# Kernel tuning notes

Measured on AMD Instinct MI355X. Metric: run time of the kernel, lower is better.

Reference implementation:

```python
import jax, jax.numpy as jnp
import numpy as np

NUM_HEADS = 16


def setup_inputs() -> dict:
    key = jax.random.key(0)
    ks = jax.random.split(key, 5)
    B, N, C = 4, 2048, 1024
    x = jax.random.normal(ks[0], (B, N, C), dtype=jnp.float32)
    mask = jax.random.randint(ks[1], (B, N), 0, 2, dtype=jnp.int32)
    W_qkv = jax.random.normal(ks[2], (C, 3 * C), dtype=jnp.float32) * (C ** -0.5)
    W_proj = jax.random.normal(ks[3], (C, C), dtype=jnp.float32) * (C ** -0.5)
    b_proj = jnp.zeros((C,), dtype=jnp.float32)
    return {"x": x, "mask": mask, "W_qkv": W_qkv, "W_proj": W_proj, "b_proj": b_proj}


def reference(x, mask, W_qkv, W_proj, b_proj):
    B, N, C = x.shape
    H = NUM_HEADS
    hd = C // H
    scale = hd ** -0.5
    # qkv projection -> [3, B, H, N, hd]
    qkv = (x @ W_qkv).reshape(B, N, 3, H, hd).transpose(2, 0, 3, 1, 4)
    q, k, v = qkv[0], qkv[1], qkv[2]
    attn = jnp.einsum('bhqd,bhkd->bhqk', q, k) * scale  # [B,H,N,N]
    add_mask = (mask[:, None, None, :] != 1).astype(jnp.float32) * -10000.0
    attn = jax.nn.softmax(attn + add_mask, axis=-1)
    out = jnp.einsum('bhqk,bhkd->bhqd', attn, v)  # [B,H,N,hd]
    out = out.transpose(0, 2, 1, 3).reshape(B, N, C)
    return out @ W_proj + b_proj
```

## Files before the change

### kernel.cpp

```cpp
#include <hip/hip_runtime.h>

typedef unsigned short u16;
typedef unsigned int u32;
typedef unsigned long long u64;
typedef __attribute__((ext_vector_type(8))) short short8;
typedef __attribute__((ext_vector_type(4))) float f32x4;

#define MLOGC (-14426.95f)

__device__ __forceinline__ u16 f2bf(float f) {
  u32 u = __builtin_bit_cast(u32, f);
  u += 0x7fffu + ((u >> 16) & 1u);
  return (u16)(u >> 16);
}

__device__ __forceinline__ float fexp2(float x) {
#if __has_builtin(__builtin_amdgcn_exp2f)
  return __builtin_amdgcn_exp2f(x);
#else
  return exp2f(x);
#endif
}

__device__ __forceinline__ void glds16(u16* lds, const u16* g) {
  __builtin_amdgcn_global_load_lds(
      (const __attribute__((address_space(1))) u32*)g,
      (__attribute__((address_space(3))) u32*)lds, 16, 0, 0);
}

#define MFMA(a, b, c) __builtin_amdgcn_mfma_f32_16x16x32_bf16((a), (b), (c), 0, 0, 0)


__global__ __launch_bounds__(256) void prep(const float* __restrict__ x,
                                            const int* __restrict__ mask,
                                            const float* __restrict__ Wqkv,
                                            const float* __restrict__ Wproj,
                                            u16* __restrict__ xb,
                                            u16* __restrict__ wqkvt,
                                            u16* __restrict__ wprojt,
                                            int* __restrict__ s2t,
                                            int* __restrict__ nkbuf) {
  __shared__ float tile[64][65];
  __shared__ int wtot[4];
  __shared__ int wbase[5];
  const int bid = blockIdx.x, t = threadIdx.x;

  if (bid < 8192) {
    int i = bid * 256 + t;
    float4 v = ((const float4*)x)[i];
    union { u16 s[4]; u64 ll; } u;
    u.s[0] = f2bf(v.x); u.s[1] = f2bf(v.y); u.s[2] = f2bf(v.z); u.s[3] = f2bf(v.w);
    ((u64*)xb)[i] = u.ll;
    return;
  }
  if (bid < 9216) {
    const float* Wm; u16* Wt; int Cc, bj, bi;
    if (bid < 8960) { int tt = bid - 8192; Wm = Wqkv;  Wt = wqkvt;  Cc = 3072; bj = tt % 48; bi = tt / 48; }
    else            { int tt = bid - 8960; Wm = Wproj; Wt = wprojt; Cc = 1024; bj = tt & 15; bi = tt >> 4; }
    const int r = t >> 4, c4 = (t & 15) << 2;
    for (int rr = r; rr < 64; rr += 16) {
      float4 v = *(const float4*)&Wm[(size_t)(bi * 64 + rr) * Cc + bj * 64 + c4];
      tile[rr][c4] = v.x; tile[rr][c4 + 1] = v.y; tile[rr][c4 + 2] = v.z; tile[rr][c4 + 3] = v.w;
    }
    __syncthreads();
    for (int rr = r; rr < 64; rr += 16) {
      union { u16 s[4]; u64 ll; } u;
      u.s[0] = f2bf(tile[c4][rr]);
      u.s[1] = f2bf(tile[c4 + 1][rr]);
      u.s[2] = f2bf(tile[c4 + 2][rr]);
      u.s[3] = f2bf(tile[c4 + 3][rr]);
      *(u64*)&Wt[(size_t)(bj * 64 + rr) * 1024 + bi * 64 + c4] = u.ll;
    }
    return;
  }
  const int b = bid - 9216;
  const int lane = t & 63, w = t >> 6;
  int m8[8], c = 0;
  #pragma unroll
  for (int j = 0; j < 8; j++) {
    m8[j] = (mask[b * 2048 + t * 8 + j] == 1);
    c += m8[j];
  }
  int incl = c;
  #pragma unroll
  for (int off = 1; off < 64; off <<= 1) {
    int v = __shfl_up(incl, off);
    if (lane >= off) incl += v;
  }
  if (lane == 63) wtot[w] = incl;
  __syncthreads();
  if (t == 0) {
    int s = 0;
    for (int i = 0; i < 4; i++) { wbase[i] = s; s += wtot[i]; }
    wbase[4] = s;
  }
  __syncthreads();
  const int nk = wbase[4];
  int urun = wbase[w] + incl - c;
  #pragma unroll
  for (int j = 0; j < 8; j++) {
    int tok = t * 8 + j;
    int slot = m8[j] ? urun : nk + (tok - urun);
    s2t[b * 2048 + slot] = b * 2048 + tok;
    urun += m8[j];
  }
  if (t == 0) nkbuf[b] = nk;
}

__global__ __launch_bounds__(256, 4) void gemm_fused(const u16* __restrict__ xb,
                                                     const u16* __restrict__ wqkvt,
                                                     const int* __restrict__ s2t,
                                                     const int* __restrict__ nkbuf,
                                                     u16* __restrict__ qbuf,
                                                     u16* __restrict__ kc,
                                                     u16* __restrict__ vtc) {
  __shared__ u16 Asm[128 * 64];
  __shared__ u16 Bsm[128 * 64];
  const int bid = blockIdx.x;
  const int role = bid >> 9;
  const int sub = bid & 511;
  const int tid = threadIdx.x, lane = tid & 63, w = tid >> 6;
  const int quad = lane >> 4, l15 = lane & 15;
  const int wm = (w >> 1) * 64, wn = (w & 1) * 64;
  const int srow = lane >> 3;
  const int gcc = ((lane & 7) ^ srow) * 8;
  const int rx8 = (l15 & 7);

  int m0, n0;
  const u16 *Asrc, *Bsrc;
  if (role == 2) { m0 = (sub & 7) * 128; n0 = (sub >> 3) * 128; }
  else           { m0 = (sub >> 3) * 128; n0 = (sub & 7) * 128; }
  if (role == 1 && (m0 & 2047) >= nkbuf[m0 >> 11]) return;
  if (role == 2 && (n0 & 2047) >= nkbuf[n0 >> 11]) return;

  int arow[4], brow[4];
  #pragma unroll
  for (int c = 0; c < 4; ++c) {
    int rit = (w * 4 + c) * 8 + srow;
    if (role == 0)      { arow[c] = m0 + rit;            brow[c] = n0 + rit; }
    else if (role == 1) { arow[c] = s2t[m0 + rit];       brow[c] = 1024 + n0 + rit; }
    else                { arow[c] = 2048 + m0 + rit;     brow[c] = s2t[n0 + rit]; }
  }
  Asrc = (role == 2) ? wqkvt : xb;
  Bsrc = (role == 2) ? xb : wqkvt;

  f32x4 acc[4][4];
  #pragma unroll
  for (int i = 0; i < 4; i++)
    #pragma unroll
    for (int j = 0; j < 4; j++)
      #pragma unroll
      for (int r = 0; r < 4; r++) acc[i][j][r] = 0.f;

  for (int kt = 0; kt < 1024; kt += 64) {
    __syncthreads();
    #pragma unroll
    for (int c = 0; c < 4; ++c) {
      int chunk = w * 4 + c;
      glds16(&Asm[chunk * 512], &Asrc[(size_t)arow[c] * 1024 + kt + gcc]);
      glds16(&Bsm[chunk * 512], &Bsrc[(size_t)brow[c] * 1024 + kt + gcc]);
    }
    __syncthreads();
    #pragma unroll
    for (int ks = 0; ks < 2; ++ks) {
      int pc = ((ks * 4 + quad) ^ rx8) * 8;
      short8 av[4], bv[4];
      #pragma unroll
      for (int i = 0; i < 4; i++)
        av[i] = *(const short8*)&Asm[(wm + i * 16 + l15) * 64 + pc];
      #pragma unroll
      for (int j = 0; j < 4; j++)
        bv[j] = *(const short8*)&Bsm[(wn + j * 16 + l15) * 64 + pc];
      #pragma unroll
      for (int i = 0; i < 4; i++)
        #pragma unroll
        for (int j = 0; j < 4; j++)
          acc[i][j] = MFMA(av[i], bv[j], acc[i][j]);
    }
  }

  if (role == 2) {
    #pragma unroll
    for (int j = 0; j < 4; j++) {
      int col = n0 + wn + j * 16 + l15;
      int bb = col >> 11, sl = col & 2047;
      #pragma unroll
      for (int i = 0; i < 4; i++)
        #pragma unroll
        for (int r = 0; r < 4; r++) {
          int row = m0 + wm + i * 16 + quad * 4 + r;
          vtc[(size_t)(bb * 1024 + row) * 2048 + sl] = f2bf(acc[i][j][r]);
        }
    }
  } else {
    u16* dst = (role == 0) ? qbuf : kc;
    #pragma unroll
    for (int i = 0; i < 4; i++)
      #pragma unroll
      for (int j = 0; j < 4; j++) {
        int col = n0 + wn + j * 16 + l15;
        #pragma unroll
        for (int r = 0; r < 4; r++) {
          int row = m0 + wm + i * 16 + quad * 4 + r;
          dst[(size_t)row * 1024 + col] = f2bf(acc[i][j][r]);
        }
      }
  }
}

__global__ __launch_bounds__(256, 2) void attn_kernel(const u16* __restrict__ q,
                                                      const u16* __restrict__ kc,
                                                      const u16* __restrict__ vtc,
                                                      const int* __restrict__ nkbuf,
                                                      u16* __restrict__ ao) {
  __shared__ u16 Ksm[64 * 64];
  __shared__ u16 Vsm[64 * 64];
  __shared__ u16 Psm[4 * 64 * 72];
  const int h = blockIdx.x, b = blockIdx.y, qt = blockIdx.z;
  const int tid = threadIdx.x, lane = tid & 63, w = tid >> 6;
  const int quad = lane >> 4, l15 = lane & 15;
  const int q0 = qt * 256 + w * 64;
  const int srow = lane >> 3;
  const int gcc = ((lane & 7) ^ srow) * 8;
  const int rx8 = (l15 & 7);
  const float C1 = 0.18033688f;
  const int nk = nkbuf[b];
  const int ntiles = (nk + 63) >> 6;

  short8 qf[4][2];
  #pragma unroll
  for (int i = 0; i < 4; i++)
    #pragma unroll
    for (int ks = 0; ks < 2; ks++)
      qf[i][ks] = *(const short8*)&q[(size_t)(b * 2048 + q0 + i * 16 + l15) * 1024 +
                                     h * 64 + ks * 32 + quad * 8];

  f32x4 o[4][4];
  float lsum[4][4];
  #pragma unroll
  for (int i = 0; i < 4; i++)
    #pragma unroll
    for (int r = 0; r < 4; r++) {
      lsum[i][r] = 0.f;
      #pragma unroll
      for (int jd = 0; jd < 4; jd++) o[i][jd][r] = 0.f;
    }

  for (int t = 0; t < ntiles; ++t) {
    const int k0 = t * 64;
    __syncthreads();
    #pragma unroll
    for (int c = 0; c < 2; ++c) {
      int chunk = w * 2 + c;
      int r = chunk * 8 + srow;
      glds16(&Ksm[chunk * 512], &kc[(size_t)(b * 2048 + k0 + r) * 1024 + h * 64 + gcc]);
      glds16(&Vsm[chunk * 512], &vtc[(size_t)(b * 1024 + h * 64 + r) * 2048 + k0 + gcc]);
    }
    __syncthreads();

    f32x4 s[4][4];
    #pragma unroll
    for (int i = 0; i < 4; i++)
      #pragma unroll
      for (int j = 0; j < 4; j++)
        #pragma unroll
        for (int r = 0; r < 4; r++) s[i][j][r] = 0.f;
    #pragma unroll
    for (int ks = 0; ks < 2; ks++) {
      int pc = ((ks * 4 + quad) ^ rx8) * 8;
      short8 kf[4];
      #pragma unroll
      for (int j = 0; j < 4; j++)
        kf[j] = *(const short8*)&Ksm[(j * 16 + l15) * 64 + pc];
      #pragma unroll
      for (int i = 0; i < 4; i++)
        #pragma unroll
        for (int j = 0; j < 4; j++) s[i][j] = MFMA(qf[i][ks], kf[j], s[i][j]);
    }

    float mlog[4];
    #pragma unroll
    for (int j = 0; j < 4; j++)
      mlog[j] = (k0 + j * 16 + l15 < nk) ? 0.f : MLOGC;

    #pragma unroll
    for (int i = 0; i < 4; i++) {
      #pragma unroll
      for (int r = 0; r < 4; r++) {
        int prow = i * 16 + quad * 4 + r;
        float ps = 0.f;
        #pragma unroll
        for (int j = 0; j < 4; j++) {
          float p = fexp2(__builtin_fmaf(s[i][j][r], C1, mlog[j]));
          ps += p;
          u32 pv = __builtin_bit_cast(u32, p) + 0x8000u;
          Psm[w * 4608 + prow * 72 + j * 16 + l15] = ((const u16*)&pv)[1];
        }
        lsum[i][r] += ps;
      }
    }

    #pragma unroll
    for (int ks = 0; ks < 2; ks++) {
      int pcv = ((ks * 4 + quad) ^ rx8) * 8;
      int kk = ks * 32 + quad * 8;
      short8 pf[4], vf[4];
      #pragma unroll
      for (int i = 0; i < 4; i++)
        pf[i] = *(const short8*)&Psm[w * 4608 + (i * 16 + l15) * 72 + kk];
      #pragma unroll
      for (int jd = 0; jd < 4; jd++)
        vf[jd] = *(const short8*)&Vsm[(jd * 16 + l15) * 64 + pcv];
      #pragma unroll
      for (int i = 0; i < 4; i++)
        #pragma unroll
        for (int jd = 0; jd < 4; jd++) o[i][jd] = MFMA(pf[i], vf[jd], o[i][jd]);
    }
  }

  #pragma unroll
  for (int i = 0; i < 4; i++)
    #pragma unroll
    for (int r = 0; r < 4; r++) {
      float l = lsum[i][r];
      #pragma unroll
      for (int off = 8; off >= 1; off >>= 1) l += __shfl_xor(l, off);
      float inv = 1.f / l;
      size_t row = (size_t)(b * 2048 + q0 + i * 16 + quad * 4 + r);
      #pragma unroll
      for (int jd = 0; jd < 4; jd++)
        ao[row * 1024 + h * 64 + jd * 16 + l15] = f2bf(o[i][jd][r] * inv);
    }
}

__global__ __launch_bounds__(256, 3) void gemm_proj(const u16* __restrict__ A,
                                                    const u16* __restrict__ Bt,
                                                    const float* __restrict__ bias,
                                                    float* __restrict__ out) {
  __shared__ u16 Asm[128 * 64];
  __shared__ u16 Bsm[128 * 64];
  const int tid = threadIdx.x, lane = tid & 63, w = tid >> 6;
  const int quad = lane >> 4, l15 = lane & 15;
  const int m0 = blockIdx.y * 128, n0 = blockIdx.x * 128;
  const int wm = (w >> 1) * 64, wn = (w & 1) * 64;
  const int srow = lane >> 3;
  const int gcc = ((lane & 7) ^ srow) * 8;
  const int rx8 = (l15 & 7);
  f32x4 acc[4][4];
  #pragma unroll
  for (int i = 0; i < 4; i++)
    #pragma unroll
    for (int j = 0; j < 4; j++)
      #pragma unroll
      for (int r = 0; r < 4; r++) acc[i][j][r] = 0.f;

  for (int kt = 0; kt < 1024; kt += 64) {
    __syncthreads();
    #pragma unroll
    for (int c = 0; c < 4; ++c) {
      int chunk = w * 4 + c;
      int row = chunk * 8 + srow;
      glds16(&Asm[chunk * 512], &A[(size_t)(m0 + row) * 1024 + kt + gcc]);
      glds16(&Bsm[chunk * 512], &Bt[(size_t)(n0 + row) * 1024 + kt + gcc]);
    }
    __syncthreads();
    #pragma unroll
    for (int ks = 0; ks < 2; ++ks) {
      int pc = ((ks * 4 + quad) ^ rx8) * 8;
      short8 av[4], bv[4];
      #pragma unroll
      for (int i = 0; i < 4; i++)
        av[i] = *(const short8*)&Asm[(wm + i * 16 + l15) * 64 + pc];
      #pragma unroll
      for (int j = 0; j < 4; j++)
        bv[j] = *(const short8*)&Bsm[(wn + j * 16 + l15) * 64 + pc];
      #pragma unroll
      for (int i = 0; i < 4; i++)
        #pragma unroll
        for (int j = 0; j < 4; j++)
          acc[i][j] = MFMA(av[i], bv[j], acc[i][j]);
    }
  }

  #pragma unroll
  for (int j = 0; j < 4; j++) {
    int col = n0 + wn + j * 16 + l15;
    float bj = bias[col];
    #pragma unroll
    for (int i = 0; i < 4; i++) {
      #pragma unroll
      for (int r = 0; r < 4; r++) {
        int row = m0 + wm + i * 16 + quad * 4 + r;
        out[(size_t)row * 1024 + col] = acc[i][j][r] + bj;
      }
    }
  }
}

extern "C" void kernel_launch(void* const* d_in, const int* in_sizes, int n_in,
                              void* d_out, int out_size, void* d_ws, size_t ws_size,
                              hipStream_t stream) {
  (void)in_sizes; (void)n_in; (void)out_size; (void)ws_size;
  const float* x     = (const float*)d_in[0];
  const int*   mask  = (const int*)d_in[1];
  const float* Wqkv  = (const float*)d_in[2];
  const float* Wproj = (const float*)d_in[3];
  const float* bproj = (const float*)d_in[4];
  float* out = (float*)d_out;
  char* ws = (char*)d_ws;

  size_t off = 0;
  u16* xb     = (u16*)(ws + off); off += 8192ull * 1024 * 2;
  u16* wqkvt  = (u16*)(ws + off); off += 3072ull * 1024 * 2;
  u16* wprojt = (u16*)(ws + off); off += 1024ull * 1024 * 2;
  u16* qbuf   = (u16*)(ws + off); off += 8192ull * 1024 * 2;
  u16* kcbuf  = (u16*)(ws + off); off += 4096ull * 2048 * 2;
  u16* vtcbuf = (u16*)(ws + off); off += 4096ull * 2048 * 2;
  u16* aobuf  = (u16*)(ws + off); off += 8192ull * 1024 * 2;
  int* s2t    = (int*)(ws + off); off += 8192ull * 4;
  int* nkbuf  = (int*)(ws + off); off += 4 * 4;

  prep<<<9220, 256, 0, stream>>>(x, mask, Wqkv, Wproj, xb, wqkvt, wprojt, s2t, nkbuf);
  gemm_fused<<<1536, 256, 0, stream>>>(xb, wqkvt, s2t, nkbuf, qbuf, kcbuf, vtcbuf);
  attn_kernel<<<dim3(16, 4, 8), 256, 0, stream>>>(qbuf, kcbuf, vtcbuf, nkbuf, aobuf);
  gemm_proj<<<dim3(8, 64), 256, 0, stream>>>(aobuf, wprojt, bproj, out);
}
```

Baseline: 232.0 us.

## Compute S transposed and keep P in registers, dropping the LDS round trip

The QK^T MFMA now takes K as the A operand, so each lane holds scores for one query column. K rows are loaded into LDS in a permuted order so that the resulting register layout matches the B-operand layout the PV MFMA expects. The probabilities are packed to bf16 with perm instructions and fed straight to the PV MFMA. This removes the Psm shared buffer, its stores and its reloads. Masking is skipped for full key tiles, and the row-sum reduction changes to match the new layout, at the cost of extra index arithmetic and a dependence on the permuted row ordering being exactly right.

```diff
diff --git a/kernel.cpp b/kernel.cpp
--- a/kernel.cpp
+++ b/kernel.cpp
@@ -215,7 +215,6 @@
                                                       u16* __restrict__ ao) {
   __shared__ u16 Ksm[64 * 64];
   __shared__ u16 Vsm[64 * 64];
-  __shared__ u16 Psm[4 * 64 * 72];
   const int h = blockIdx.x, b = blockIdx.y, qt = blockIdx.z;
   const int tid = threadIdx.x, lane = tid & 63, w = tid >> 6;
   const int quad = lane >> 4, l15 = lane & 15;
@@ -226,6 +225,15 @@
   const float C1 = 0.18033688f;
   const int nk = nkbuf[b];
   const int ntiles = (nk + 63) >> 6;
+  const int quad8 = quad * 8;
+
+  int vrow[2], prow[2];
+  #pragma unroll
+  for (int c = 0; c < 2; ++c) {
+    int row = (w * 2 + c) * 8 + srow;
+    vrow[c] = row;
+    prow[c] = ((row >> 4) & 1) * 32 + ((row >> 2) & 3) * 8 + ((row >> 5) & 1) * 4 + (row & 3);
+  }
 
   short8 qf[4][2];
   #pragma unroll
@@ -236,15 +244,15 @@
                                      h * 64 + ks * 32 + quad * 8];
 
   f32x4 o[4][4];
-  float lsum[4][4];
-  #pragma unroll
-  for (int i = 0; i < 4; i++)
-    #pragma unroll
-    for (int r = 0; r < 4; r++) {
-      lsum[i][r] = 0.f;
-      #pragma unroll
-      for (int jd = 0; jd < 4; jd++) o[i][jd][r] = 0.f;
-    }
+  float lsum[4];
+  #pragma unroll
+  for (int i = 0; i < 4; i++) {
+    lsum[i] = 0.f;
+    #pragma unroll
+    for (int jd = 0; jd < 4; jd++)
+      #pragma unroll
+      for (int r = 0; r < 4; r++) o[i][jd][r] = 0.f;
+  }
 
   for (int t = 0; t < ntiles; ++t) {
     const int k0 = t * 64;
@@ -252,19 +260,18 @@
     #pragma unroll
     for (int c = 0; c < 2; ++c) {
       int chunk = w * 2 + c;
-      int r = chunk * 8 + srow;
-      glds16(&Ksm[chunk * 512], &kc[(size_t)(b * 2048 + k0 + r) * 1024 + h * 64 + gcc]);
-      glds16(&Vsm[chunk * 512], &vtc[(size_t)(b * 1024 + h * 64 + r) * 2048 + k0 + gcc]);
+      glds16(&Ksm[chunk * 512], &kc[(size_t)(b * 2048 + k0 + prow[c]) * 1024 + h * 64 + gcc]);
+      glds16(&Vsm[chunk * 512], &vtc[(size_t)(b * 1024 + h * 64 + vrow[c]) * 2048 + k0 + gcc]);
     }
     __syncthreads();
 
     f32x4 s[4][4];
     #pragma unroll
-    for (int i = 0; i < 4; i++)
-      #pragma unroll
-      for (int j = 0; j < 4; j++)
-        #pragma unroll
-        for (int r = 0; r < 4; r++) s[i][j][r] = 0.f;
+    for (int j = 0; j < 4; j++)
+      #pragma unroll
+      for (int i = 0; i < 4; i++)
+        #pragma unroll
+        for (int r = 0; r < 4; r++) s[j][i][r] = 0.f;
     #pragma unroll
     for (int ks = 0; ks < 2; ks++) {
       int pc = ((ks * 4 + quad) ^ rx8) * 8;
@@ -273,59 +280,85 @@
       for (int j = 0; j < 4; j++)
         kf[j] = *(const short8*)&Ksm[(j * 16 + l15) * 64 + pc];
       #pragma unroll
-      for (int i = 0; i < 4; i++)
-        #pragma unroll
-        for (int j = 0; j < 4; j++) s[i][j] = MFMA(qf[i][ks], kf[j], s[i][j]);
-    }
-
-    float mlog[4];
-    #pragma unroll
-    for (int j = 0; j < 4; j++)
-      mlog[j] = (k0 + j * 16 + l15 < nk) ? 0.f : MLOGC;
-
+      for (int j = 0; j < 4; j++)
+        #pragma unroll
+        for (int i = 0; i < 4; i++) s[j][i] = MFMA(kf[j], qf[i][ks], s[j][i]);
+    }
+
+    float mlog[4][4];
+    if (k0 + 64 <= nk) {
+      #pragma unroll
+      for (int j = 0; j < 4; j++)
+        #pragma unroll
+        for (int r = 0; r < 4; r++) mlog[j][r] = 0.f;
+    } else {
+      #pragma unroll
+      for (int j = 0; j < 4; j++)
+        #pragma unroll
+        for (int r = 0; r < 4; r++) {
+          int slot = k0 + (j & 1) * 32 + quad8 + (j >> 1) * 4 + r;
+          mlog[j][r] = (slot < nk) ? 0.f : MLOGC;
+        }
+    }
+
+    short8 pf[4][2];
     #pragma unroll
     for (int i = 0; i < 4; i++) {
-      #pragma unroll
-      for (int r = 0; r < 4; r++) {
-        int prow = i * 16 + quad * 4 + r;
-        float ps = 0.f;
-        #pragma unroll
-        for (int j = 0; j < 4; j++) {
-          float p = fexp2(__builtin_fmaf(s[i][j][r], C1, mlog[j]));
-          ps += p;
-          u32 pv = __builtin_bit_cast(u32, p) + 0x8000u;
-          Psm[w * 4608 + prow * 72 + j * 16 + l15] = ((const u16*)&pv)[1];
+      float p[4][4];
+      float ps = 0.f;
+      #pragma unroll
+      for (int j = 0; j < 4; j++)
+        #pragma unroll
+        for (int r = 0; r < 4; r++) {
+          p[j][r] = fexp2(__builtin_fmaf(s[j][i][r], C1, mlog[j][r]));
+          ps += p[j][r];
         }
-        lsum[i][r] += ps;
+      lsum[i] += ps;
+      #pragma unroll
+      for (int ks = 0; ks < 2; ks++) {
+        union { u32 u[4]; short8 v; } pk;
+        u32 a0 = __builtin_bit_cast(u32, p[ks][0]) + 0x8000u;
+        u32 a1 = __builtin_bit_cast(u32, p[ks][1]) + 0x8000u;
+        u32 a2 = __builtin_bit_cast(u32, p[ks][2]) + 0x8000u;
+        u32 a3 = __builtin_bit_cast(u32, p[ks][3]) + 0x8000u;
+        u32 b0 = __builtin_bit_cast(u32, p[ks + 2][0]) + 0x8000u;
+        u32 b1 = __builtin_bit_cast(u32, p[ks + 2][1]) + 0x8000u;
+        u32 b2 = __builtin_bit_cast(u32, p[ks + 2][2]) + 0x8000u;
+        u32 b3 = __builtin_bit_cast(u32, p[ks + 2][3]) + 0x8000u;
+        pk.u[0] = __builtin_amdgcn_perm(a1, a0, 0x07060302u);
+        pk.u[1] = __builtin_amdgcn_perm(a3, a2, 0x07060302u);
+        pk.u[2] = __builtin_amdgcn_perm(b1, b0, 0x07060302u);
+        pk.u[3] = __builtin_amdgcn_perm(b3, b2, 0x07060302u);
+        pf[i][ks] = pk.v;
       }
     }
 
     #pragma unroll
     for (int ks = 0; ks < 2; ks++) {
       int pcv = ((ks * 4 + quad) ^ rx8) * 8;
-      int kk = ks * 32 + quad * 8;
-      short8 pf[4], vf[4];
-      #pragma unroll
-      for (int i = 0; i < 4; i++)
-        pf[i] = *(const short8*)&Psm[w * 4608 + (i * 16 + l15) * 72 + kk];
+      short8 vf[4];
       #pragma unroll
       for (int jd = 0; jd < 4; jd++)
         vf[jd] = *(const short8*)&Vsm[(jd * 16 + l15) * 64 + pcv];
       #pragma unroll
       for (int i = 0; i < 4; i++)
         #pragma unroll
-        for (int jd = 0; jd < 4; jd++) o[i][jd] = MFMA(pf[i], vf[jd], o[i][jd]);
-    }
-  }
-
+        for (int jd = 0; jd < 4; jd++) o[i][jd] = MFMA(pf[i][ks], vf[jd], o[i][jd]);
+    }
+  }
+
+  #pragma unroll
+  for (int i = 0; i < 4; i++) {
+    float l = lsum[i];
+    l += __shfl_xor(l, 16);
+    l += __shfl_xor(l, 32);
+    lsum[i] = l;
+  }
   #pragma unroll
   for (int i = 0; i < 4; i++)
     #pragma unroll
     for (int r = 0; r < 4; r++) {
-      float l = lsum[i][r];
-      #pragma unroll
-      for (int off = 8; off >= 1; off >>= 1) l += __shfl_xor(l, off);
-      float inv = 1.f / l;
+      float inv = 1.f / __shfl(lsum[i], (lane & 48) | (quad * 4 + r));
       size_t row = (size_t)(b * 2048 + q0 + i * 16 + quad * 4 + r);
       #pragma unroll
       for (int jd = 0; jd < 4; jd++)
```

New measurement: 225.7 us. 2.7% less time.

## Keep softmax probabilities in registers and compute row sums via MFMA

Applied to the files above, without the earlier changes.

The attention kernel now computes S transposed (K·Q), so the exponentiated scores land in registers already in the layout needed for the P·V MFMA operand. They are packed to bf16 with perm instructions instead of being written to and read back from the LDS P buffer. The softmax scale is folded into Q at projection time. Row sums are computed by an extra MFMA against a ones vector, which removes the shuffle reduction. K rows are loaded with a permuted row order to match the new P layout, and two 64-key tiles are loaded per barrier. Risks are the extra MFMA work for the sums and correctness of the row permutation and tail masking. The aobuf workspace now aliases xb.

```diff
diff --git a/kernel.cpp b/kernel.cpp
--- a/kernel.cpp
+++ b/kernel.cpp
@@ -6,7 +6,7 @@
 typedef __attribute__((ext_vector_type(8))) short short8;
 typedef __attribute__((ext_vector_type(4))) float f32x4;
 
-#define MLOGC (-14426.95f)
+#define QSCALE 0.18033688f
 
 __device__ __forceinline__ u16 f2bf(float f) {
   u32 u = __builtin_bit_cast(u32, f);
@@ -194,6 +194,7 @@
     }
   } else {
     u16* dst = (role == 0) ? qbuf : kc;
+    const float sc = (role == 0) ? QSCALE : 1.f;
     #pragma unroll
     for (int i = 0; i < 4; i++)
       #pragma unroll
@@ -202,7 +203,7 @@
         #pragma unroll
         for (int r = 0; r < 4; r++) {
           int row = m0 + wm + i * 16 + quad * 4 + r;
-          dst[(size_t)row * 1024 + col] = f2bf(acc[i][j][r]);
+          dst[(size_t)row * 1024 + col] = f2bf(acc[i][j][r] * sc);
         }
       }
   }
@@ -213,9 +214,8 @@
                                                       const u16* __restrict__ vtc,
                                                       const int* __restrict__ nkbuf,
                                                       u16* __restrict__ ao) {
-  __shared__ u16 Ksm[64 * 64];
-  __shared__ u16 Vsm[64 * 64];
-  __shared__ u16 Psm[4 * 64 * 72];
+  __shared__ u16 Ksm[2][64 * 64];
+  __shared__ u16 Vsm[2][64 * 64];
   const int h = blockIdx.x, b = blockIdx.y, qt = blockIdx.z;
   const int tid = threadIdx.x, lane = tid & 63, w = tid >> 6;
   const int quad = lane >> 4, l15 = lane & 15;
@@ -223,9 +223,21 @@
   const int srow = lane >> 3;
   const int gcc = ((lane & 7) ^ srow) * 8;
   const int rx8 = (l15 & 7);
-  const float C1 = 0.18033688f;
   const int nk = nkbuf[b];
-  const int ntiles = (nk + 63) >> 6;
+  const int nt2 = (nk + 127) >> 7;
+  const int quad8 = quad * 8;
+
+  int vrow[2], prow[2];
+  #pragma unroll
+  for (int c = 0; c < 2; ++c) {
+    int row = (w * 2 + c) * 8 + srow;
+    vrow[c] = row;
+    prow[c] = ((row >> 4) & 1) * 32 + ((row >> 2) & 3) * 8 + ((row >> 5) & 1) * 4 + (row & 3);
+  }
+
+  short8 ones;
+  #pragma unroll
+  for (int z = 0; z < 8; z++) ones[z] = (short)0x3F80;
 
   short8 qf[4][2];
   #pragma unroll
@@ -235,97 +247,105 @@
       qf[i][ks] = *(const short8*)&q[(size_t)(b * 2048 + q0 + i * 16 + l15) * 1024 +
                                      h * 64 + ks * 32 + quad * 8];
 
-  f32x4 o[4][4];
-  float lsum[4][4];
-  #pragma unroll
-  for (int i = 0; i < 4; i++)
-    #pragma unroll
-    for (int r = 0; r < 4; r++) {
-      lsum[i][r] = 0.f;
-      #pragma unroll
-      for (int jd = 0; jd < 4; jd++) o[i][jd][r] = 0.f;
-    }
-
-  for (int t = 0; t < ntiles; ++t) {
-    const int k0 = t * 64;
+  f32x4 o[4][4], osum[4];
+  #pragma unroll
+  for (int i = 0; i < 4; i++) {
+    #pragma unroll
+    for (int r = 0; r < 4; r++) osum[i][r] = 0.f;
+    #pragma unroll
+    for (int jd = 0; jd < 4; jd++)
+      #pragma unroll
+      for (int r = 0; r < 4; r++) o[i][jd][r] = 0.f;
+  }
+
+#define SUBTILE(st_, kbase_)                                                           \
+  {                                                                                    \
+    f32x4 s[4][4];                                                                     \
+    _Pragma("unroll") for (int j = 0; j < 4; j++)                                      \
+      _Pragma("unroll") for (int i = 0; i < 4; i++)                                    \
+        _Pragma("unroll") for (int r = 0; r < 4; r++) s[j][i][r] = 0.f;                \
+    _Pragma("unroll") for (int ks = 0; ks < 2; ks++) {                                 \
+      int pc = ((ks * 4 + quad) ^ rx8) * 8;                                            \
+      short8 kf[4];                                                                    \
+      _Pragma("unroll") for (int j = 0; j < 4; j++)                                    \
+        kf[j] = *(const short8*)&Ksm[st_][(j * 16 + l15) * 64 + pc];                   \
+      _Pragma("unroll") for (int j = 0; j < 4; j++)                                    \
+        _Pragma("unroll") for (int i = 0; i < 4; i++)                                  \
+          s[j][i] = MFMA(kf[j], qf[i][ks], s[j][i]);                                   \
+    }                                                                                  \
+    const bool tail = ((kbase_) + 64 > nk);                                            \
+    short8 pf[4][2];                                                                   \
+    _Pragma("unroll") for (int i = 0; i < 4; i++) {                                    \
+      float p[4][4];                                                                   \
+      if (!tail) {                                                                     \
+        _Pragma("unroll") for (int j = 0; j < 4; j++)                                  \
+          _Pragma("unroll") for (int r = 0; r < 4; r++)                                \
+            p[j][r] = fexp2(s[j][i][r]);                                               \
+      } else {                                                                         \
+        _Pragma("unroll") for (int j = 0; j < 4; j++)                                  \
+          _Pragma("unroll") for (int r = 0; r < 4; r++) {                              \
+            int slot = (kbase_) + (j & 1) * 32 + quad8 + (j >> 1) * 4 + r;             \
+            float e = fexp2(s[j][i][r]);                                               \
+            p[j][r] = (slot < nk) ? e : 0.f;                                           \
+          }                                                                            \
+      }                                                                                \
+      _Pragma("unroll") for (int ks = 0; ks < 2; ks++) {                               \
+        union { u32 u[4]; short8 v; } pk;                                              \
+        u32 a0 = __builtin_bit_cast(u32, p[ks][0]) + 0x8000u;                          \
+        u32 a1 = __builtin_bit_cast(u32, p[ks][1]) + 0x8000u;                          \
+        u32 a2 = __builtin_bit_cast(u32, p[ks][2]) + 0x8000u;                          \
+        u32 a3 = __builtin_bit_cast(u32, p[ks][3]) + 0x8000u;                          \
+        u32 b0 = __builtin_bit_cast(u32, p[ks + 2][0]) + 0x8000u;                      \
+        u32 b1 = __builtin_bit_cast(u32, p[ks + 2][1]) + 0x8000u;                      \
+        u32 b2 = __builtin_bit_cast(u32, p[ks + 2][2]) + 0x8000u;                      \
+        u32 b3 = __builtin_bit_cast(u32, p[ks + 2][3]) + 0x8000u;                      \
+        pk.u[0] = __builtin_amdgcn_perm(a1, a0, 0x07060302u);                          \
+        pk.u[1] = __builtin_amdgcn_perm(a3, a2, 0x07060302u);                          \
+        pk.u[2] = __builtin_amdgcn_perm(b1, b0, 0x07060302u);                          \
+        pk.u[3] = __builtin_amdgcn_perm(b3, b2, 0x07060302u);                          \
+        pf[i][ks] = pk.v;                                                              \
+      }                                                                                \
+    }                                                                                  \
+    _Pragma("unroll") for (int ks = 0; ks < 2; ks++) {                                 \
+      int pcv = ((ks * 4 + quad) ^ rx8) * 8;                                           \
+      short8 vf[4];                                                                    \
+      _Pragma("unroll") for (int jd = 0; jd < 4; jd++)                                 \
+        vf[jd] = *(const short8*)&Vsm[st_][(jd * 16 + l15) * 64 + pcv];                \
+      _Pragma("unroll") for (int i = 0; i < 4; i++) {                                  \
+        osum[i] = MFMA(pf[i][ks], ones, osum[i]);                                      \
+        _Pragma("unroll") for (int jd = 0; jd < 4; jd++)                               \
+          o[i][jd] = MFMA(pf[i][ks], vf[jd], o[i][jd]);                                \
+      }                                                                                \
+    }                                                                                  \
+  }
+
+  for (int t = 0; t < nt2; ++t) {
+    const int k0 = t * 128;
     __syncthreads();
     #pragma unroll
     for (int c = 0; c < 2; ++c) {
       int chunk = w * 2 + c;
-      int r = chunk * 8 + srow;
-      glds16(&Ksm[chunk * 512], &kc[(size_t)(b * 2048 + k0 + r) * 1024 + h * 64 + gcc]);
-      glds16(&Vsm[chunk * 512], &vtc[(size_t)(b * 1024 + h * 64 + r) * 2048 + k0 + gcc]);
-    }
-    __syncthreads();
-
-    f32x4 s[4][4];
-    #pragma unroll
-    for (int i = 0; i < 4; i++)
-      #pragma unroll
-      for (int j = 0; j < 4; j++)
-        #pragma unroll
-        for (int r = 0; r < 4; r++) s[i][j][r] = 0.f;
-    #pragma unroll
-    for (int ks = 0; ks < 2; ks++) {
-      int pc = ((ks * 4 + quad) ^ rx8) * 8;
-      short8 kf[4];
-      #pragma unroll
-      for (int j = 0; j < 4; j++)
-        kf[j] = *(const short8*)&Ksm[(j * 16 + l15) * 64 + pc];
-      #pragma unroll
-      for (int i = 0; i < 4; i++)
-        #pragma unroll
-        for (int j = 0; j < 4; j++) s[i][j] = MFMA(qf[i][ks], kf[j], s[i][j]);
-    }
-
-    float mlog[4];
-    #pragma unroll
-    for (int j = 0; j < 4; j++)
-      mlog[j] = (k0 + j * 16 + l15 < nk) ? 0.f : MLOGC;
-
-    #pragma unroll
-    for (int i = 0; i < 4; i++) {
-      #pragma unroll
-      for (int r = 0; r < 4; r++) {
-        int prow = i * 16 + quad * 4 + r;
-        float ps = 0.f;
-        #pragma unroll
-        for (int j = 0; j < 4; j++) {
-          float p = fexp2(__builtin_fmaf(s[i][j][r], C1, mlog[j]));
-          ps += p;
-          u32 pv = __builtin_bit_cast(u32, p) + 0x8000u;
-          Psm[w * 4608 + prow * 72 + j * 16 + l15] = ((const u16*)&pv)[1];
-        }
-        lsum[i][r] += ps;
-      }
-    }
-
-    #pragma unroll
-    for (int ks = 0; ks < 2; ks++) {
-      int pcv = ((ks * 4 + quad) ^ rx8) * 8;
-      int kk = ks * 32 + quad * 8;
-      short8 pf[4], vf[4];
-      #pragma unroll
-      for (int i = 0; i < 4; i++)
-        pf[i] = *(const short8*)&Psm[w * 4608 + (i * 16 + l15) * 72 + kk];
-      #pragma unroll
-      for (int jd = 0; jd < 4; jd++)
-        vf[jd] = *(const short8*)&Vsm[(jd * 16 + l15) * 64 + pcv];
-      #pragma unroll
-      for (int i = 0; i < 4; i++)
-        #pragma unroll
-        for (int jd = 0; jd < 4; jd++) o[i][jd] = MFMA(pf[i], vf[jd], o[i][jd]);
-    }
-  }
+      glds16(&Ksm[0][chunk * 512],
+             &kc[(size_t)(b * 2048 + k0 + prow[c]) * 1024 + h * 64 + gcc]);
+      glds16(&Vsm[0][chunk * 512],
+             &vtc[(size_t)(b * 1024 + h * 64 + vrow[c]) * 2048 + k0 + gcc]);
+      glds16(&Ksm[1][chunk * 512],
+             &kc[(size_t)(b * 2048 + k0 + 64 + prow[c]) * 1024 + h * 64 + gcc]);
+      glds16(&Vsm[1][chunk * 512],
+             &vtc[(size_t)(b * 1024 + h * 64 + vrow[c]) * 2048 + k0 + 64 + gcc]);
+    }
+    __syncthreads();
+
+    SUBTILE(0, k0)
+    if (k0 + 64 < nk) SUBTILE(1, k0 + 64)
+  }
+#undef SUBTILE
 
   #pragma unroll
   for (int i = 0; i < 4; i++)
     #pragma unroll
     for (int r = 0; r < 4; r++) {
-      float l = lsum[i][r];
-      #pragma unroll
-      for (int off = 8; off >= 1; off >>= 1) l += __shfl_xor(l, off);
-      float inv = 1.f / l;
+      float inv = 1.f / osum[i][r];
       size_t row = (size_t)(b * 2048 + q0 + i * 16 + quad * 4 + r);
       #pragma unroll
       for (int jd = 0; jd < 4; jd++)
@@ -416,9 +436,9 @@
   u16* qbuf   = (u16*)(ws + off); off += 8192ull * 1024 * 2;
   u16* kcbuf  = (u16*)(ws + off); off += 4096ull * 2048 * 2;
   u16* vtcbuf = (u16*)(ws + off); off += 4096ull * 2048 * 2;
-  u16* aobuf  = (u16*)(ws + off); off += 8192ull * 1024 * 2;
   int* s2t    = (int*)(ws + off); off += 8192ull * 4;
   int* nkbuf  = (int*)(ws + off); off += 4 * 4;
+  u16* aobuf  = xb;
 
   prep<<<9220, 256, 0, stream>>>(x, mask, Wqkv, Wproj, xb, wqkvt, wprojt, s2t, nkbuf);
   gemm_fused<<<1536, 256, 0, stream>>>(xb, wqkvt, s2t, nkbuf, qbuf, kcbuf, vtcbuf);
```

Result: faster. 217.9 us (-6.1%).
